# Optimization experiments

Measured on AMD Instinct MI355X. Metric: run time of the kernel, lower is better.

The kernel has to match this reference:

```python
import jax, jax.numpy as jnp
import numpy as np

N_NODES = 100000
N_EDGES = 3200000

def setup_inputs() -> dict:
    key = jax.random.key(0)
    ks = jax.random.split(key, 16)
    x = jax.random.normal(ks[0], (N_NODES, 3), dtype=jnp.float32)
    edge_index = jax.random.randint(ks[1], (2, N_EDGES), 0, N_NODES, dtype=jnp.int32)
    def glorot(k, shape):
        fan = shape[0] + shape[-1]
        lim = jnp.sqrt(6.0 / fan)
        return jax.random.uniform(k, shape, jnp.float32, -lim, lim)
    params = {
        'W1': glorot(ks[2], (3, 32)),  'as1': glorot(ks[3], (2, 16)), 'ad1': glorot(ks[4], (2, 16)), 'b1': jnp.zeros((32,), jnp.float32),
        'W2': glorot(ks[5], (32, 32)), 'as2': glorot(ks[6], (2, 16)), 'ad2': glorot(ks[7], (2, 16)), 'b2': jnp.zeros((32,), jnp.float32),
        'W3': glorot(ks[8], (32, 8)),  'as3': glorot(ks[9], (1, 8)),  'ad3': glorot(ks[10], (1, 8)), 'b3': jnp.zeros((8,), jnp.float32),
        'Wo': glorot(ks[11], (8, 1)),  'bo': jnp.zeros((1,), jnp.float32),
    }
    return dict(x=x, edge_index=edge_index, **params)

def _gat_layer(x, src, dst, W, a_src, a_dst, bias, n_heads, c_out):
    # PyG GATConv: linear -> per-head attention logits -> leaky_relu -> segment softmax over dst -> scatter-weighted sum -> concat heads + bias
    N = x.shape[0]
    h = (x @ W).reshape(N, n_heads, c_out)              # [N,H,C]
    al_s = jnp.sum(h * a_src[None], axis=-1)            # [N,H]
    al_d = jnp.sum(h * a_dst[None], axis=-1)            # [N,H]
    logits = jax.nn.leaky_relu(al_s[src] + al_d[dst], 0.2)  # [E,H]
    m = jax.ops.segment_max(logits, dst, num_segments=N)
    e = jnp.exp(logits - m[dst])
    s = jax.ops.segment_sum(e, dst, num_segments=N)
    alpha = e / (s[dst] + 1e-16)                        # [E,H]
    msg = h[src] * alpha[:, :, None]                    # [E,H,C]
    out = jax.ops.segment_sum(msg, dst, num_segments=N) # [N,H,C]
    return out.reshape(N, n_heads * c_out) + bias

def reference(x, edge_index, W1, as1, ad1, b1, W2, as2, ad2, b2, W3, as3, ad3, b3, Wo, bo):
    N = x.shape[0]
    # add self loops (PyG GATConv default add_self_loops=True)
    loop = jnp.arange(N, dtype=edge_index.dtype)
    src = jnp.concatenate([edge_index[0], loop])
    dst = jnp.concatenate([edge_index[1], loop])
    h = jax.nn.elu(_gat_layer(x, src, dst, W1, as1, ad1, b1, 2, 16))
    h = jax.nn.elu(_gat_layer(h, src, dst, W2, as2, ad2, b2, 2, 16))
    h = jax.nn.elu(_gat_layer(h, src, dst, W3, as3, ad3, b3, 1, 8))
    return h @ Wo + bo
```

## Files before the change

### kernel.cpp

```cpp
#include <hip/hip_runtime.h>
#include <hip/hip_bf16.h>
#include <math.h>

#define DEVINL __device__ __forceinline__

DEVINL float loadIn(const void* p, long i, int bf) {
    return bf ? __bfloat162float(((const __hip_bfloat16*)p)[i])
              : ((const float*)p)[i];
}

DEVINL float leaky(float v) { return fmaxf(v, 0.2f * v); }

DEVINL unsigned pack_bf16(float a, float b) {
    __hip_bfloat16 x = __float2bfloat16(a), y = __float2bfloat16(b);
    unsigned short ux = *reinterpret_cast<unsigned short*>(&x);
    unsigned short uy = *reinterpret_cast<unsigned short*>(&y);
    return (unsigned)ux | ((unsigned)uy << 16);
}
DEVINL float lo16(unsigned u) { return __uint_as_float(u << 16); }
DEVINL float hi16(unsigned u) { return __uint_as_float(u & 0xFFFF0000u); }

__global__ __launch_bounds__(1024) void prep(const unsigned* __restrict__ x,
                                             int* __restrict__ flag,
                                             int* __restrict__ bcnt) {
    __shared__ int sh[1024];
    int t = threadIdx.x;
    bcnt[t] = 0;
    int cnt = 0;
    for (int i = t; i < 2048; i += 1024) {
        unsigned ex = (x[i] >> 7) & 0xFFu;
        if (ex >= 110u && ex <= 140u) cnt++;
    }
    sh[t] = cnt;
    __syncthreads();
    for (int s = 512; s > 0; s >>= 1) {
        if (t < s) sh[t] += sh[t + s];
        __syncthreads();
    }
    if (t == 0) *flag = (sh[0] >= 1200) ? 1 : 0;
}

__global__ __launch_bounds__(256) void bhist(const int* __restrict__ dst, int E,
                                             int* __restrict__ bcnt) {
    __shared__ int lh[512];
    for (int i = threadIdx.x; i < 512; i += 256) lh[i] = 0;
    __syncthreads();
    int stride = gridDim.x * 256;
    for (int e = blockIdx.x * 256 + threadIdx.x; e < E; e += stride)
        atomicAdd(&lh[dst[e] >> 8], 1);
    __syncthreads();
    for (int i = threadIdx.x; i < 512; i += 256)
        if (lh[i]) atomicAdd(&bcnt[i], lh[i]);
}

__global__ __launch_bounds__(1024) void bscan(const int* __restrict__ bcnt,
                                              int* __restrict__ bstart,
                                              int* __restrict__ bcur) {
    __shared__ int sA[1024], sB[1024];
    int t = threadIdx.x;
    int c = bcnt[t];
    sA[t] = c;
    __syncthreads();
    int* a = sA; int* b = sB;
    for (int off = 1; off < 1024; off <<= 1) {
        int v = a[t] + ((t >= off) ? a[t - off] : 0);
        __syncthreads();
        b[t] = v;
        __syncthreads();
        int* tp = a; a = b; b = tp;
    }
    int excl = a[t] - c;
    bstart[t] = excl;
    bcur[t] = excl;
    if (t == 1023) bstart[1024] = a[t];
}

#define CS_CHUNK 16384
__global__ __launch_bounds__(512) void block_scatter(
    const int* __restrict__ srcIdx, const int* __restrict__ dstIdx, int E,
    int* __restrict__ bcur, int* __restrict__ buf) {
    __shared__ int lh[512];
    __shared__ int lcur[512];
    int t = threadIdx.x;
    int e0 = blockIdx.x * CS_CHUNK;
    int e1 = e0 + CS_CHUNK; if (e1 > E) e1 = E;

    if (t < 512) lh[t] = 0;
    __syncthreads();
    for (int e = e0 + t; e < e1; e += 512)
        atomicAdd(&lh[dstIdx[e] >> 8], 1);
    __syncthreads();
    if (t < 512) {
        int c = lh[t];
        lcur[t] = c ? atomicAdd(&bcur[t], c) : 0;
    }
    __syncthreads();
    for (int e = e0 + t; e < e1; e += 512) {
        int d = dstIdx[e];
        int s = srcIdx[e];
        int pos = atomicAdd(&lcur[d >> 8], 1);
        buf[pos] = ((d & 255) << 17) | s;
    }
}

#define FS_CAP 10240
__global__ __launch_bounds__(256) void fine_scatter(
    const int* __restrict__ bstart, int* buf, int* ss,
    int* __restrict__ rp, int* __restrict__ cnt, int N) {
    __shared__ int stage[FS_CAP];
    __shared__ int hcnt[256];
    __shared__ int hA[256], hB[256];
    __shared__ int lcur[256];
    int bkt = blockIdx.x;
    int t = threadIdx.x;
    int s0 = bstart[bkt];
    int m = bstart[bkt + 1] - s0;
    if (m > FS_CAP) m = FS_CAP;

    for (int i = t; i < m; i += 256) stage[i] = buf[s0 + i];
    hcnt[t] = 0;
    __syncthreads();
    for (int i = t; i < m; i += 256) atomicAdd(&hcnt[stage[i] >> 17], 1);
    __syncthreads();
    hA[t] = hcnt[t];
    __syncthreads();
    int* a = hA; int* b = hB;
    for (int off = 1; off < 256; off <<= 1) {
        int v = a[t] + ((t >= off) ? a[t - off] : 0);
        __syncthreads();
        b[t] = v;
        __syncthreads();
        int* tp = a; a = b; b = tp;
    }
    {
        int excl = a[t] - hcnt[t];
        lcur[t] = s0 + excl;
        int node = bkt * 256 + t;
        if (node < N) {
            rp[node] = s0 + excl;
            cnt[node] = hcnt[t];
        }
    }
    __syncthreads();
    for (int i = t; i < m; i += 256) {
        int v = stage[i];
        int pos = atomicAdd(&lcur[v >> 17], 1);
        ss[pos] = v & 0x1FFFF;
    }
}

__global__ __launch_bounds__(256) void xprep(
    const void* __restrict__ x, const int* __restrict__ flagp,
    const void* __restrict__ W1, const void* __restrict__ as1,
    const void* __restrict__ ad1,
    float4* __restrict__ xp, float* __restrict__ cvec, int N)
{
    const int bf = *flagp;
    int n = blockIdx.x * 256 + threadIdx.x;
    if (n < N) {
        float4 v;
        v.x = loadIn(x, (long)n * 3 + 0, bf);
        v.y = loadIn(x, (long)n * 3 + 1, bf);
        v.z = loadIn(x, (long)n * 3 + 2, bf);
        v.w = 0.0f;
        xp[n] = v;
    }
    if (blockIdx.x == 0 && threadIdx.x < 12) {
        int t = threadIdx.x;
        int isd = t >= 6;
        int h = (t - 6 * isd) / 3;
        int k = (t - 6 * isd) % 3;
        const void* av = isd ? ad1 : as1;
        float s = 0.0f;
        for (int c = 0; c < 16; c++)
            s += loadIn(W1, k * 32 + h * 16 + c, bf) * loadIn(av, h * 16 + c, bf);
        cvec[t] = s;
    }
}

__global__ __launch_bounds__(256) void aggregate_l1(
    const int* __restrict__ rp_start, const int* __restrict__ cnt,
    const int* __restrict__ ss, const float4* __restrict__ xp,
    const float* __restrict__ cvec,
    const void* __restrict__ W1, const void* __restrict__ b1,
    const int* __restrict__ flagp,
    unsigned* __restrict__ xout, int N)
{
    const int bf = *flagp;
    __shared__ float Wl[96];
    __shared__ float bl[32];
    for (int i = threadIdx.x; i < 96; i += 256) Wl[i] = loadIn(W1, i, bf);
    for (int i = threadIdx.x; i < 32; i += 256) bl[i] = loadIn(b1, i, bf);
    __syncthreads();

    int lane = threadIdx.x & 63;
    int g = lane >> 4;
    int q = lane & 15;
    int wid = threadIdx.x >> 6;

    float cs[2][3], cd[2][3];
#pragma unroll
    for (int h = 0; h < 2; h++)
#pragma unroll
        for (int k = 0; k < 3; k++) {
            cs[h][k] = cvec[h * 3 + k];
            cd[h][k] = cvec[6 + h * 3 + k];
        }

    const int nstride = gridDim.x * 16;
    for (int node = blockIdx.x * 16 + wid * 4 + g; ; node += nstride) {
        if (node - g >= N) break;
        bool valid = node < N;
        int idx = valid ? node : 0;
        int start = rp_start[idx];
        int deg = valid ? cnt[idx] : 0;
        float4 xn = xp[idx];

        float alsn[2], aldn[2];
#pragma unroll
        for (int h = 0; h < 2; h++) {
            alsn[h] = xn.x * cs[h][0] + xn.y * cs[h][1] + xn.z * cs[h][2];
            aldn[h] = xn.x * cd[h][0] + xn.y * cd[h][1] + xn.z * cd[h][2];
        }

        float a00 = 0.f, a01 = 0.f, a02 = 0.f, s0 = 0.f;
        float a10 = 0.f, a11 = 0.f, a12 = 0.f, s1 = 0.f;

        if (q == 0 && valid) {
            float e0 = __expf(fminf(leaky(alsn[0] + aldn[0]), 80.0f));
            float e1 = __expf(fminf(leaky(alsn[1] + aldn[1]), 80.0f));
            a00 = e0 * xn.x; a01 = e0 * xn.y; a02 = e0 * xn.z; s0 = e0;
            a10 = e1 * xn.x; a11 = e1 * xn.y; a12 = e1 * xn.z; s1 = e1;
        }

        for (int kb = q; kb < deg; kb += 32) {
            int k2 = kb + 16;
            bool ok2 = k2 < deg;
            int sA = ss[start + kb];
            int sB = ss[start + (ok2 ? k2 : kb)];
            float4 xa = xp[sA];
            float4 xb = xp[sB];
            {
                float l0 = xa.x * cs[0][0] + xa.y * cs[0][1] + xa.z * cs[0][2] + aldn[0];
                float l1 = xa.x * cs[1][0] + xa.y * cs[1][1] + xa.z * cs[1][2] + aldn[1];
                float e0 = __expf(fminf(leaky(l0), 80.0f));
                float e1 = __expf(fminf(leaky(l1), 80.0f));
                a00 = fmaf(xa.x, e0, a00); a01 = fmaf(xa.y, e0, a01);
                a02 = fmaf(xa.z, e0, a02); s0 += e0;
                a10 = fmaf(xa.x, e1, a10); a11 = fmaf(xa.y, e1, a11);
                a12 = fmaf(xa.z, e1, a12); s1 += e1;
            }
            {
                float l0 = xb.x * cs[0][0] + xb.y * cs[0][1] + xb.z * cs[0][2] + aldn[0];
                float l1 = xb.x * cs[1][0] + xb.y * cs[1][1] + xb.z * cs[1][2] + aldn[1];
                float e0 = ok2 ? __expf(fminf(leaky(l0), 80.0f)) : 0.0f;
                float e1 = ok2 ? __expf(fminf(leaky(l1), 80.0f)) : 0.0f;
                a00 = fmaf(xb.x, e0, a00); a01 = fmaf(xb.y, e0, a01);
                a02 = fmaf(xb.z, e0, a02); s0 += e0;
                a10 = fmaf(xb.x, e1, a10); a11 = fmaf(xb.y, e1, a11);
                a12 = fmaf(xb.z, e1, a12); s1 += e1;
            }
        }

#pragma unroll
        for (int off = 1; off < 16; off <<= 1) {
            a00 += __shfl_xor(a00, off, 64); a01 += __shfl_xor(a01, off, 64);
            a02 += __shfl_xor(a02, off, 64); s0  += __shfl_xor(s0,  off, 64);
            a10 += __shfl_xor(a10, off, 64); a11 += __shfl_xor(a11, off, 64);
            a12 += __shfl_xor(a12, off, 64); s1  += __shfl_xor(s1,  off, 64);
        }

        if (valid) {
            int h = q >> 3;
            float inv = 1.0f / ((h ? s1 : s0) + 1e-16f);
            float g0 = (h ? a10 : a00) * inv;
            float g1 = (h ? a11 : a01) * inv;
            float g2 = (h ? a12 : a02) * inv;
            int c0 = 2 * q;
            float v0 = g0 * Wl[c0]      + g1 * Wl[32 + c0]      + g2 * Wl[64 + c0]      + bl[c0];
            float v1 = g0 * Wl[c0 + 1]  + g1 * Wl[32 + c0 + 1]  + g2 * Wl[64 + c0 + 1]  + bl[c0 + 1];
            v0 = v0 > 0.0f ? v0 : __expf(fminf(v0, 0.0f)) - 1.0f;
            v1 = v1 > 0.0f ? v1 : __expf(fminf(v1, 0.0f)) - 1.0f;
            xout[(long)node * 16 + q] = pack_bf16(v0, v1);
        }
    }
}

template <int XMODE, int C_IN, int H, int C>
__global__ __launch_bounds__(256) void node_transform(
    const void* __restrict__ xin, const int* __restrict__ flagp,
    const void* __restrict__ W, const void* __restrict__ a_s,
    const void* __restrict__ a_d,
    unsigned* __restrict__ h2, float* __restrict__ als,
    float* __restrict__ ald, int N)
{
    const int bf = *flagp;
    constexpr int HC = H * C;
    __shared__ float Ws[C_IN * HC];
    __shared__ float asS[HC];
    __shared__ float adS[HC];
    for (int i = threadIdx.x; i < C_IN * HC; i += 256) Ws[i] = loadIn(W, i, bf);
    for (int i = threadIdx.x; i < HC; i += 256) {
        asS[i] = loadIn(a_s, i, bf);
        adS[i] = loadIn(a_d, i, bf);
    }
    __syncthreads();

    int n = blockIdx.x * 256 + threadIdx.x;
    if (n >= N) return;

    float xv[C_IN];
    if (XMODE) {
        const uint4* x4 = (const uint4*)xin;
#pragma unroll
        for (int q = 0; q < C_IN / 8; q++) {
            uint4 w = x4[(long)n * (C_IN / 8) + q];
            xv[q * 8 + 0] = lo16(w.x); xv[q * 8 + 1] = hi16(w.x);
            xv[q * 8 + 2] = lo16(w.y); xv[q * 8 + 3] = hi16(w.y);
            xv[q * 8 + 4] = lo16(w.z); xv[q * 8 + 5] = hi16(w.z);
            xv[q * 8 + 6] = lo16(w.w); xv[q * 8 + 7] = hi16(w.w);
        }
    } else {
#pragma unroll
        for (int k = 0; k < C_IN; k++) xv[k] = loadIn(xin, (long)n * C_IN + k, bf);
    }

    float hv[HC];
#pragma unroll
    for (int j = 0; j < HC; j++) {
        float v = 0.0f;
#pragma unroll
        for (int k = 0; k < C_IN; k++) v = fmaf(xv[k], Ws[k * HC + j], v);
        hv[j] = v;
    }
#pragma unroll
    for (int jj = 0; jj < HC / 2; jj++)
        h2[(long)n * (HC / 2) + jj] = pack_bf16(hv[2 * jj], hv[2 * jj + 1]);

#pragma unroll
    for (int hh = 0; hh < H; hh++) {
        float vs = 0.0f, vd = 0.0f;
#pragma unroll
        for (int c = 0; c < C; c++) {
            vs = fmaf(hv[hh * C + c], asS[hh * C + c], vs);
            vd = fmaf(hv[hh * C + c], adS[hh * C + c], vd);
        }
        als[(long)n * H + hh] = vs;
        ald[(long)n * H + hh] = vd;
    }
}

template <int H, int C, int NCH, int UNR, int FUSE>
__global__ __launch_bounds__(256) void aggregate(
    const int* __restrict__ rp_start, const int* __restrict__ cnt,
    const int* __restrict__ ss,
    const unsigned* __restrict__ h2,
    const float* __restrict__ als, const float* __restrict__ ald,
    const void* __restrict__ bias, const void* __restrict__ Wo,
    const void* __restrict__ bo, const int* __restrict__ flagp,
    void* __restrict__ xout, int N)
{
    constexpr int HC = H * C;
    constexpr int J = HC / NCH;
    constexpr int EPW = 64 / J;
    const int bf = *flagp;
    int lane = threadIdx.x & 63;
    int p = lane / J;
    int j = lane % J;
    int c0 = NCH * j;
    int head = c0 / C;
    const float* __restrict__ alsH = als + head;

    float bv[NCH];
#pragma unroll
    for (int i = 0; i < NCH; i++) bv[i] = loadIn(bias, c0 + i, bf);
    float wov[NCH];
    float bov = 0.0f;
    if constexpr (FUSE) {
#pragma unroll
        for (int i = 0; i < NCH; i++) wov[i] = loadIn(Wo, c0 + i, bf);
        bov = loadIn(bo, 0, bf);
    }

    const int nstride = gridDim.x << 2;
    for (int node = (blockIdx.x << 2) + (threadIdx.x >> 6); node < N;
         node += nstride) {

        int start = rp_start[node];
        int deg = cnt[node];
        int degm1 = deg - 1;
        float ald_n = ald[node * H + head];

        float acc[NCH];
        float ssum = 0.0f;
#pragma unroll
        for (int i = 0; i < NCH; i++) acc[i] = 0.0f;

        if (p == 0) {
            float es = __expf(fminf(leaky(alsH[node * H] + ald_n), 80.0f));
            if constexpr (NCH == 4) {
                uint2 hv = ((const uint2*)h2)[node * (HC / 4) + j];
                acc[0] = lo16(hv.x) * es; acc[1] = hi16(hv.x) * es;
                acc[2] = lo16(hv.y) * es; acc[3] = hi16(hv.y) * es;
            } else {
                unsigned hv = h2[node * (HC / 2) + j];
                acc[0] = lo16(hv) * es; acc[1] = hi16(hv) * es;
            }
            ssum = es;
        }

        for (int kb = p; kb < deg; kb += UNR * EPW) {
            int srcs[UNR];
            bool ok[UNR];
#pragma unroll
            for (int u = 0; u < UNR; u++) {
                int k = kb + u * EPW;
                ok[u] = (k < deg);
                int kc = ok[u] ? k : degm1;
                srcs[u] = ss[start + kc];
            }
            float av[UNR];
            uint2 hv4[UNR];
            unsigned hv2[UNR];
#pragma unroll
            for (int u = 0; u < UNR; u++) {
                av[u] = alsH[srcs[u] * H];
                if constexpr (NCH == 4)
                    hv4[u] = ((const uint2*)h2)[srcs[u] * (HC / 4) + j];
                else
                    hv2[u] = h2[srcs[u] * (HC / 2) + j];
            }
#pragma unroll
            for (int u = 0; u < UNR; u++) {
                float e = ok[u] ? __expf(fminf(leaky(av[u] + ald_n), 80.0f)) : 0.0f;
                if constexpr (NCH == 4) {
                    acc[0] = fmaf(lo16(hv4[u].x), e, acc[0]);
                    acc[1] = fmaf(hi16(hv4[u].x), e, acc[1]);
                    acc[2] = fmaf(lo16(hv4[u].y), e, acc[2]);
                    acc[3] = fmaf(hi16(hv4[u].y), e, acc[3]);
                } else {
                    acc[0] = fmaf(lo16(hv2[u]), e, acc[0]);
                    acc[1] = fmaf(hi16(hv2[u]), e, acc[1]);
                }
                ssum += e;
            }
        }

#pragma unroll
        for (int off = J; off < 64; off <<= 1) {
#pragma unroll
            for (int i = 0; i < NCH; i++) acc[i] += __shfl_xor(acc[i], off, 64);
            ssum += __shfl_xor(ssum, off, 64);
        }

        float inv = 1.0f / (ssum + 1e-16f);
        float v[NCH];
#pragma unroll
        for (int i = 0; i < NCH; i++) {
            float t = acc[i] * inv + bv[i];
            float en = __expf(fminf(t, 0.0f)) - 1.0f;
            v[i] = t > 0.0f ? t : en;
        }

        if (FUSE) {
            float r = 0.0f;
#pragma unroll
            for (int i = 0; i < NCH; i++) r = fmaf(v[i], wov[i], r);
#pragma unroll
            for (int off = 1; off < J; off <<= 1) r += __shfl_xor(r, off, 64);
            if (lane == 0) {
                r += bov;
                if (bf) ((__hip_bfloat16*)xout)[node] = __float2bfloat16(r);
                else    ((float*)xout)[node] = r;
            }
        } else {
            if (p == 0) {
                if constexpr (NCH == 4) {
                    uint2 o; o.x = pack_bf16(v[0], v[1]); o.y = pack_bf16(v[2], v[3]);
                    ((uint2*)xout)[node * (HC / 4) + j] = o;
                } else {
                    ((unsigned*)xout)[node * (HC / 2) + j] = pack_bf16(v[0], v[1]);
                }
            }
        }
    }
}

extern "C" void kernel_launch(void* const* d_in, const int* in_sizes, int n_in,
                              void* d_out, int out_size, void* d_ws, size_t ws_size,
                              hipStream_t stream) {
    const void* x   = d_in[0];
    const int*  ei  = (const int*)d_in[1];
    const void* W1  = d_in[2];
    const void* as1 = d_in[3];
    const void* ad1 = d_in[4];
    const void* b1  = d_in[5];
    const void* W2  = d_in[6];
    const void* as2 = d_in[7];
    const void* ad2 = d_in[8];
    const void* b2  = d_in[9];
    const void* W3  = d_in[10];
    const void* as3 = d_in[11];
    const void* ad3 = d_in[12];
    const void* b3  = d_in[13];
    const void* Wo  = d_in[14];
    const void* bo  = d_in[15];

    const int N = in_sizes[0] / 3;
    const int E = in_sizes[1] / 2;
    const int* ei0 = ei;
    const int* ei1 = ei + E;

    int* flag   = (int*)d_ws;
    int* bcnt   = flag + 64;
    int* bstart = bcnt + 1024;
    int* bcur   = bstart + 1088;
    int* cnt    = bcur + 1024;
    int* rp     = cnt + N;
    int* ss     = rp + N;
    float* als  = (float*)(ss + E);
    float* ald  = als + (long)N * 2;
    unsigned* A = (unsigned*)(ald + (long)N * 2);
    unsigned* h = A + (long)N * 16;
    float4* xp  = (float4*)(h + (long)N * 16);
    float* cvec = (float*)(xp + (long)N);

    const int B = 256;
    auto cdiv = [](long a, long b) { return (int)((a + b - 1) / b); };
    const int NBKT = cdiv(N, 256);

    const int aggBlocks = 2048;

    prep<<<1, 1024, 0, stream>>>((const unsigned*)x, flag, bcnt);
    xprep<<<cdiv(N, B), B, 0, stream>>>(x, flag, W1, as1, ad1, xp, cvec, N);
    bhist<<<256, B, 0, stream>>>(ei1, E, bcnt);
    bscan<<<1, 1024, 0, stream>>>(bcnt, bstart, bcur);
    block_scatter<<<cdiv(E, CS_CHUNK), 512, 0, stream>>>(ei0, ei1, E, bcur, ss);
    fine_scatter<<<NBKT, B, 0, stream>>>(bstart, ss, ss, rp, cnt, N);

    aggregate_l1<<<aggBlocks, B, 0, stream>>>(
        rp, cnt, ss, xp, cvec, W1, b1, flag, A, N);

    node_transform<1, 32, 2, 16><<<cdiv(N, B), B, 0, stream>>>(
        A, flag, W2, as2, ad2, h, als, ald, N);
    aggregate<2, 16, 4, 6, 0><<<aggBlocks, B, 0, stream>>>(
        rp, cnt, ss, h, als, ald, b2, flag ? nullptr : nullptr, nullptr, flag, A, N);

    node_transform<1, 32, 1, 8><<<cdiv(N, B), B, 0, stream>>>(
        A, flag, W3, as3, ad3, h, als, ald, N);
    aggregate<1, 8, 2, 3, 1><<<aggBlocks, B, 0, stream>>>(
        rp, cnt, ss, h, als, ald, b3, Wo, bo, flag, d_out, N);
}
```

Baseline: 323.2 us.

## Software-pipeline aggregate kernel across nodes with double-buffered CSR and gather loads

Restructures the aggregate node loop into a two-stage software pipeline. The CSR row info, self features and the first UNR*EPW neighbor indices and gathers for the next node(s) are issued while the current node's math and reduction run. Nodes with degree above the prefetched slot count fall back to a simple tail loop. The goal is to hide dependent-load latency (index then gather) across nodes, at the cost of more registers and macro-heavy code.

```diff
diff --git a/kernel.cpp b/kernel.cpp
--- a/kernel.cpp
+++ b/kernel.cpp
@@ -363,6 +363,7 @@
     constexpr int HC = H * C;
     constexpr int J = HC / NCH;
     constexpr int EPW = 64 / J;
+    constexpr int SLOTS = UNR * EPW;
     const int bf = *flagp;
     int lane = threadIdx.x & 63;
     int p = lane / J;
@@ -383,107 +384,150 @@
     }
 
     const int nstride = gridDim.x << 2;
-    for (int node = (blockIdx.x << 2) + (threadIdx.x >> 6); node < N;
-         node += nstride) {
-
-        int start = rp_start[node];
-        int deg = cnt[node];
-        int degm1 = deg - 1;
-        float ald_n = ald[node * H + head];
-
-        float acc[NCH];
-        float ssum = 0.0f;
-#pragma unroll
-        for (int i = 0; i < NCH; i++) acc[i] = 0.0f;
-
-        if (p == 0) {
-            float es = __expf(fminf(leaky(alsH[node * H] + ald_n), 80.0f));
-            if constexpr (NCH == 4) {
-                uint2 hv = ((const uint2*)h2)[node * (HC / 4) + j];
-                acc[0] = lo16(hv.x) * es; acc[1] = hi16(hv.x) * es;
-                acc[2] = lo16(hv.y) * es; acc[3] = hi16(hv.y) * es;
-            } else {
-                unsigned hv = h2[node * (HC / 2) + j];
-                acc[0] = lo16(hv) * es; acc[1] = hi16(hv) * es;
-            }
-            ssum = es;
-        }
-
-        for (int kb = p; kb < deg; kb += UNR * EPW) {
-            int srcs[UNR];
-            bool ok[UNR];
-#pragma unroll
-            for (int u = 0; u < UNR; u++) {
-                int k = kb + u * EPW;
-                ok[u] = (k < deg);
-                int kc = ok[u] ? k : degm1;
-                srcs[u] = ss[start + kc];
-            }
-            float av[UNR];
-            uint2 hv4[UNR];
-            unsigned hv2[UNR];
-#pragma unroll
-            for (int u = 0; u < UNR; u++) {
-                av[u] = alsH[srcs[u] * H];
-                if constexpr (NCH == 4)
-                    hv4[u] = ((const uint2*)h2)[srcs[u] * (HC / 4) + j];
-                else
-                    hv2[u] = h2[srcs[u] * (HC / 2) + j];
-            }
-#pragma unroll
-            for (int u = 0; u < UNR; u++) {
-                float e = ok[u] ? __expf(fminf(leaky(av[u] + ald_n), 80.0f)) : 0.0f;
-                if constexpr (NCH == 4) {
-                    acc[0] = fmaf(lo16(hv4[u].x), e, acc[0]);
-                    acc[1] = fmaf(hi16(hv4[u].x), e, acc[1]);
-                    acc[2] = fmaf(lo16(hv4[u].y), e, acc[2]);
-                    acc[3] = fmaf(hi16(hv4[u].y), e, acc[3]);
-                } else {
-                    acc[0] = fmaf(lo16(hv2[u]), e, acc[0]);
-                    acc[1] = fmaf(hi16(hv2[u]), e, acc[1]);
-                }
-                ssum += e;
-            }
-        }
-
-#pragma unroll
-        for (int off = J; off < 64; off <<= 1) {
-#pragma unroll
-            for (int i = 0; i < NCH; i++) acc[i] += __shfl_xor(acc[i], off, 64);
-            ssum += __shfl_xor(ssum, off, 64);
-        }
-
-        float inv = 1.0f / (ssum + 1e-16f);
-        float v[NCH];
-#pragma unroll
-        for (int i = 0; i < NCH; i++) {
-            float t = acc[i] * inv + bv[i];
-            float en = __expf(fminf(t, 0.0f)) - 1.0f;
-            v[i] = t > 0.0f ? t : en;
-        }
-
-        if (FUSE) {
-            float r = 0.0f;
-#pragma unroll
-            for (int i = 0; i < NCH; i++) r = fmaf(v[i], wov[i], r);
-#pragma unroll
-            for (int off = 1; off < J; off <<= 1) r += __shfl_xor(r, off, 64);
-            if (lane == 0) {
-                r += bov;
-                if (bf) ((__hip_bfloat16*)xout)[node] = __float2bfloat16(r);
-                else    ((float*)xout)[node] = r;
-            }
-        } else {
-            if (p == 0) {
-                if constexpr (NCH == 4) {
-                    uint2 o; o.x = pack_bf16(v[0], v[1]); o.y = pack_bf16(v[2], v[3]);
-                    ((uint2*)xout)[node * (HC / 4) + j] = o;
-                } else {
-                    ((unsigned*)xout)[node * (HC / 2) + j] = pack_bf16(v[0], v[1]);
-                }
-            }
-        }
-    }
+    const int node0 = (blockIdx.x << 2) + (threadIdx.x >> 6);
+    if (node0 >= N) return;
+
+    int nd0, nd1, st0, st1, dg0, dg1;
+    float an0, an1, sa0, sa1;
+    uint2 sq0, sq1; unsigned sw0, sw1;
+    int sr0[UNR], sr1[UNR];
+    float av0[UNR], av1[UNR];
+    uint2 hq0[UNR], hq1[UNR];
+    unsigned hw0[UNR], hw1[UNR];
+
+#define AGG_LOADCSR(S, NODE) {                                              \
+    int nn_ = (NODE); nd##S = nn_;                                          \
+    int ii_ = nn_ < N ? nn_ : N - 1;                                        \
+    st##S = rp_start[ii_];                                                  \
+    dg##S = nn_ < N ? cnt[ii_] : 0;                                         \
+    an##S = ald[ii_ * H + head];                                            \
+    sa##S = alsH[ii_ * H];                                                  \
+    if constexpr (NCH == 4) sq##S = ((const uint2*)h2)[ii_ * (HC / 4) + j]; \
+    else sw##S = h2[ii_ * (HC / 2) + j]; }
+
+#define AGG_ISSUE_SS(S) {                                                   \
+    int dm1_ = dg##S > 0 ? dg##S - 1 : 0;                                   \
+    _Pragma("unroll") for (int u = 0; u < UNR; u++) {                       \
+        int k_ = p + u * EPW;                                               \
+        sr##S[u] = ss[st##S + (k_ < dg##S ? k_ : dm1_)]; } }
+
+#define AGG_ISSUE_G(S) {                                                    \
+    _Pragma("unroll") for (int u = 0; u < UNR; u++) {                       \
+        av##S[u] = alsH[sr##S[u] * H];                                      \
+        if constexpr (NCH == 4)                                             \
+            hq##S[u] = ((const uint2*)h2)[sr##S[u] * (HC / 4) + j];         \
+        else hw##S[u] = h2[sr##S[u] * (HC / 2) + j]; } }
+
+#define AGG_BODY(A, B) {                                                    \
+    int node_c = nd##A, start_c = st##A, deg_c = dg##A;                     \
+    float an_c = an##A, sa_c = sa##A;                                       \
+    uint2 sq_c = sq##A; unsigned sw_c = sw##A; (void)sq_c; (void)sw_c;      \
+                                             \
+    AGG_ISSUE_G(B);                                                         \
+              \
+    AGG_LOADCSR(A, node_c + 2 * nstride);                                   \
+                                                       \
+    float acc[NCH]; float ssum = 0.0f;                                      \
+    _Pragma("unroll") for (int i = 0; i < NCH; i++) acc[i] = 0.0f;          \
+    if (p == 0) {                                                           \
+        float es_ = __expf(fminf(leaky(sa_c + an_c), 80.0f));               \
+        if constexpr (NCH == 4) {                                           \
+            acc[0] = lo16(sq_c.x) * es_; acc[1] = hi16(sq_c.x) * es_;       \
+            acc[2] = lo16(sq_c.y) * es_; acc[3] = hi16(sq_c.y) * es_;       \
+        } else {                                                            \
+            acc[0] = lo16(sw_c) * es_; acc[1] = hi16(sw_c) * es_;           \
+        }                                                                   \
+        ssum = es_;                                                         \
+    }                                                                       \
+    _Pragma("unroll") for (int u = 0; u < UNR; u++) {                       \
+        int k_ = p + u * EPW;                                               \
+        float e_ = (k_ < deg_c)                                             \
+            ? __expf(fminf(leaky(av##A[u] + an_c), 80.0f)) : 0.0f;          \
+        if constexpr (NCH == 4) {                                           \
+            acc[0] = fmaf(lo16(hq##A[u].x), e_, acc[0]);                    \
+            acc[1] = fmaf(hi16(hq##A[u].x), e_, acc[1]);                    \
+            acc[2] = fmaf(lo16(hq##A[u].y), e_, acc[2]);                    \
+            acc[3] = fmaf(hi16(hq##A[u].y), e_, acc[3]);                    \
+        } else {                                                            \
+            acc[0] = fmaf(lo16(hw##A[u]), e_, acc[0]);                      \
+            acc[1] = fmaf(hi16(hw##A[u]), e_, acc[1]);                      \
+        }                                                                   \
+        ssum += e_;                                                         \
+    }                                                                       \
+                          \
+    if (deg_c > SLOTS) {                                                    \
+        for (int kb_ = SLOTS + p; kb_ < deg_c; kb_ += EPW) {                \
+            int s_ = ss[start_c + kb_];                                     \
+            float e_ = __expf(fminf(leaky(alsH[s_ * H] + an_c), 80.0f));    \
+            if constexpr (NCH == 4) {                                       \
+                uint2 hv_ = ((const uint2*)h2)[s_ * (HC / 4) + j];          \
+                acc[0] = fmaf(lo16(hv_.x), e_, acc[0]);                     \
+                acc[1] = fmaf(hi16(hv_.x), e_, acc[1]);                     \
+                acc[2] = fmaf(lo16(hv_.y), e_, acc[2]);                     \
+                acc[3] = fmaf(hi16(hv_.y), e_, acc[3]);                     \
+            } else {                                                        \
+                unsigned hv_ = h2[s_ * (HC / 2) + j];                       \
+                acc[0] = fmaf(lo16(hv_), e_, acc[0]);                       \
+                acc[1] = fmaf(hi16(hv_), e_, acc[1]);                       \
+            }                                                               \
+            ssum += e_;                                                     \
+        }                                                                   \
+    }                                                                       \
+                \
+    AGG_ISSUE_SS(A);                                                        \
+                                                        \
+    _Pragma("unroll") for (int off = J; off < 64; off <<= 1) {              \
+        _Pragma("unroll") for (int i = 0; i < NCH; i++)                     \
+            acc[i] += __shfl_xor(acc[i], off, 64);                          \
+        ssum += __shfl_xor(ssum, off, 64);                                  \
+    }                                                                       \
+    float inv = 1.0f / (ssum + 1e-16f);                                     \
+    float v[NCH];                                                           \
+    _Pragma("unroll") for (int i = 0; i < NCH; i++) {                       \
+        float t_ = acc[i] * inv + bv[i];                                    \
+        v[i] = t_ > 0.0f ? t_ : __expf(fminf(t_, 0.0f)) - 1.0f;             \
+    }                                                                       \
+    if constexpr (FUSE) {                                                   \
+        float r_ = 0.0f;                                                    \
+        _Pragma("unroll") for (int i = 0; i < NCH; i++)                     \
+            r_ = fmaf(v[i], wov[i], r_);                                    \
+        _Pragma("unroll") for (int off = 1; off < J; off <<= 1)             \
+            r_ += __shfl_xor(r_, off, 64);                                  \
+        if (lane == 0 && node_c < N) {                                      \
+            r_ += bov;                                                      \
+            if (bf) ((__hip_bfloat16*)xout)[node_c] = __float2bfloat16(r_); \
+            else    ((float*)xout)[node_c] = r_;                            \
+        }                                                                   \
+    } else {                                                                \
+        if (p == 0 && node_c < N) {                                         \
+            if constexpr (NCH == 4) {                                       \
+                uint2 o_; o_.x = pack_bf16(v[0], v[1]);                     \
+                o_.y = pack_bf16(v[2], v[3]);                               \
+                ((uint2*)xout)[node_c * (HC / 4) + j] = o_;                 \
+            } else {                                                        \
+                ((unsigned*)xout)[node_c * (HC / 2) + j] =                  \
+                    pack_bf16(v[0], v[1]);                                  \
+            }                                                               \
+        }                                                                   \
+    } }
+
+    AGG_LOADCSR(0, node0);
+    AGG_LOADCSR(1, node0 + nstride);
+    AGG_ISSUE_SS(0);
+    AGG_ISSUE_G(0);
+    AGG_ISSUE_SS(1);
+
+    for (;;) {
+        AGG_BODY(0, 1);
+        if (nd1 >= N) break;
+        AGG_BODY(1, 0);
+        if (nd0 >= N) break;
+    }
+
+#undef AGG_LOADCSR
+#undef AGG_ISSUE_SS
+#undef AGG_ISSUE_G
+#undef AGG_BODY
 }
 
 extern "C" void kernel_launch(void* const* d_in, const int* in_sizes, int n_in,
@@ -544,7 +588,7 @@
     node_transform<1, 32, 2, 16><<<cdiv(N, B), B, 0, stream>>>(
         A, flag, W2, as2, ad2, h, als, ald, N);
     aggregate<2, 16, 4, 6, 0><<<aggBlocks, B, 0, stream>>>(
-        rp, cnt, ss, h, als, ald, b2, flag ? nullptr : nullptr, nullptr, flag, A, N);
+        rp, cnt, ss, h, als, ald, b2, nullptr, nullptr, flag, A, N);
 
     node_transform<1, 32, 1, 8><<<cdiv(N, B), B, 0, stream>>>(
         A, flag, W3, as3, ad3, h, als, ald, N);
```

New measurement: 314.2 us. 1.03x faster.
